# Kernel tuning notes

Hardware: AMD Instinct MI355X
Metric: run time of the kernel (lower is better)

## Reference

```python
import jax, jax.numpy as jnp
import numpy as np

# Dims matching init_kwargs
B, S, D = 2, 2048, 1024
H, E, P, K = 8, 8, 128, 2
SCALE = 1.0 / np.sqrt(P)  # registered buffer 'scale'


def setup_inputs() -> dict:
    key = jax.random.key(0)
    ks = jax.random.split(key, 8)
    std = 1.0 / np.sqrt(D)  # reset_parameters uses std_scale/sqrt(input_size)
    return {
        "x": jax.random.normal(ks[0], (B, S, D), jnp.float32),
        "q_w": jax.random.normal(ks[1], (H * P, D), jnp.float32) * std,
        "k_w": jax.random.normal(ks[2], (H * P, D), jnp.float32) * std,
        "v_w": jax.random.normal(ks[3], (H * E, D, P), jnp.float32) * std,
        "o_w": jax.random.normal(ks[4], (H * E, P, D), jnp.float32) * (1.0 / np.sqrt(H * P)),
        "sel_v_w": jax.random.normal(ks[5], (H * E, D), jnp.float32) * std,
        "sel_o_w": jax.random.normal(ks[6], (H * E, D), jnp.float32) * std,
        "route_scale": jnp.ones((1,), jnp.float32),
    }


def _get_sel_gate(x, w, route_scale):
    """Faithful port of SwitchHeadCore.get_sel (eval mode, no bias):
    sigmoid routing logits per head, top-k expert selection, weight
    normalization, route_scale. Returned as a dense [B,S,H,E] gate so the
    indexed expert combine is expressed as a gated einsum (same math)."""
    logits = jnp.einsum('bsd,ed->bse', x, w).astype(jnp.float32)
    raw = logits.reshape(x.shape[0], x.shape[1], H, E)
    probs = jax.nn.sigmoid(raw)
    vals, idx = jax.lax.top_k(probs, K)                 # [B,S,H,K]
    vals = vals / jnp.clip(vals.sum(-1, keepdims=True), 1e-9)  # normalize_weights
    vals = vals * route_scale
    gate = (jax.nn.one_hot(idx, E, dtype=vals.dtype) * vals[..., None]).sum(-2)
    return gate  # [B,S,H,E]


def reference(x, q_w, k_w, v_w, o_w, sel_v_w, sel_o_w, route_scale):
    rs = route_scale[0]
    gate_v = _get_sel_gate(x, sel_v_w, rs)  # [B,S,H,E]
    gate_o = _get_sel_gate(x, sel_o_w, rs)  # [B,S,H,E]

    # q/k projections -> torch head order [B,H,S,P]
    q = jnp.einsum('bsd,hpd->bhsp', x, q_w.reshape(H, P, D))
    k = jnp.einsum('bsd,hpd->bhsp', x, k_w.reshape(H, P, D))

    # Per-token expert V projection: mixture of selected expert weight slices
    xv = jnp.einsum('bsd,hedp->bshep', x, v_w.reshape(H, E, D, P))
    v = jnp.einsum('bshep,bshe->bhsp', xv, gate_v)

    # Scaled dot-product attention (eval: no dropout)
    att = jax.nn.softmax(jnp.einsum('bhqp,bhkp->bhqk', q, k) * SCALE, axis=-1)
    ctx = jnp.einsum('bhqk,bhkp->bqhp', att, v)  # [B,S,H,P]

    # Per-token expert O projection, gated, summed over heads
    weighted = ctx[:, :, :, None, :] * gate_o[..., None]  # [B,S,H,E,P]
    out = jnp.einsum('bshep,hepd->bsd', weighted, o_w.reshape(H, E, P, D))
    return out
```

## Files before the change

kernel.cpp:

```cpp
#include <hip/hip_runtime.h>


typedef unsigned short u16;
typedef __attribute__((ext_vector_type(8))) short s8v;
typedef __attribute__((ext_vector_type(4))) float f4v;
typedef __attribute__((ext_vector_type(4))) unsigned short us4;

#define ATT_SCALE 0.08838834764831845f

__device__ inline u16 bf16_rne(float f) {
  union { float f; unsigned u; } v; v.f = f;
  unsigned r = v.u + 0x7fffu + ((v.u >> 16) & 1u);
  return (u16)(r >> 16);
}
__device__ inline float bf2f(u16 h) {
  union { unsigned u; float f; } v; v.u = ((unsigned)h) << 16;
  return v.f;
}

__device__ inline void glds16(const void* g, void* l) {
  __builtin_amdgcn_global_load_lds((const __attribute__((address_space(1))) void*)g,
                                   (__attribute__((address_space(3))) void*)l, 16, 0, 0);
}
__device__ inline int swzcol(int idx) {
  int r = idx >> 2;
  return (((idx & 3) ^ ((r + (r >> 2)) & 3)) << 3);
}
#define WAITB() do { asm volatile("s_waitcnt vmcnt(0)" ::: "memory"); __syncthreads(); } while (0)

__global__ void conv_qk(const float* __restrict__ Q, const float* __restrict__ K,
                        u16* __restrict__ Qb, u16* __restrict__ Kb) {
  int i = blockIdx.x * 256 + threadIdx.x;
  const float* src; u16* dst; int off;
  if (i < 262144) { src = Q; dst = Qb; off = i; }
  else            { src = K; dst = Kb; off = i - 262144; }
  float4 v = *(const float4*)&src[(size_t)off * 4];
  us4 o; o[0]=bf16_rne(v.x); o[1]=bf16_rne(v.y); o[2]=bf16_rne(v.z); o[3]=bf16_rne(v.w);
  *(us4*)&dst[(size_t)off * 4] = o;
}

__global__ void transpose_w(const float* __restrict__ src, u16* __restrict__ dst, int mode) {
  __shared__ float tile[32][33];
  int he = blockIdx.z;
  int C = mode ? 1024 : 128;
  int r0 = blockIdx.y * 32, c0 = blockIdx.x * 32;
  int lc = threadIdx.x & 31, rr = threadIdx.x >> 5;
  const float* s = src + (size_t)he * 131072;
#pragma unroll
  for (int i = 0; i < 4; ++i) {
    int r = rr + i * 8;
    tile[r][lc] = s[(size_t)(r0 + r) * C + c0 + lc];
  }
  __syncthreads();
#pragma unroll
  for (int i = 0; i < 4; ++i) {
    int c = rr + i * 8;
    float v = tile[lc][c];
    size_t a;
    if (mode) a = (size_t)(c0 + c) * 8192 + (size_t)he * 128 + (r0 + lc);
    else      a = (size_t)(he >> 3) * 1048576 + (size_t)(c0 + c) * 8192 + (size_t)(he & 7) * 1024 + (r0 + lc);
    dst[a] = bf16_rne(v);
  }
}

__global__ __launch_bounds__(256, 2) void routing(
    const float* __restrict__ X, const float* __restrict__ SelV, const float* __restrict__ SelO,
    const float* __restrict__ RS, int2* __restrict__ Tvi, float2* __restrict__ Tvg,
    int2* __restrict__ Toi, float2* __restrict__ Tog, u16* __restrict__ Xb) {
  __shared__ float xs[8][1024];
  __shared__ float lgs[8][128];
  int t0 = blockIdx.x * 8;
  int tid = threadIdx.x;
  for (int i = tid; i < 2048; i += 256) {
    int row = i >> 8, c = (i & 255) * 4;
    float4 v = *(const float4*)&X[(size_t)(t0 + row) * 1024 + c];
    *(float4*)&xs[row][c] = v;
    us4 o; o[0]=bf16_rne(v.x); o[1]=bf16_rne(v.y); o[2]=bf16_rne(v.z); o[3]=bf16_rne(v.w);
    *(us4*)&Xb[(size_t)(t0 + row) * 1024 + c] = o;
  }
  __syncthreads();
  {
    int widx = tid & 127, tg = tid >> 7;
    const float* w = (widx < 64) ? (SelV + (size_t)widx * 1024) : (SelO + (size_t)(widx - 64) * 1024);
    float acc[4] = {0.f, 0.f, 0.f, 0.f};
    for (int k = 0; k < 1024; k += 4) {
      float4 wv = *(const float4*)&w[k];
#pragma unroll
      for (int t = 0; t < 4; ++t) {
        float4 xv = *(const float4*)&xs[tg * 4 + t][k];
        acc[t] += wv.x * xv.x + wv.y * xv.y + wv.z * xv.z + wv.w * xv.w;
      }
    }
#pragma unroll
    for (int t = 0; t < 4; ++t) lgs[tg * 4 + t][widx] = acc[t];
  }
  __syncthreads();
  if (tid < 128) {
    float rs = RS[0];
    int tok = tid >> 4, which = (tid >> 3) & 1, h = tid & 7;
    float p[8];
#pragma unroll
    for (int e = 0; e < 8; ++e)
      p[e] = 1.f / (1.f + __expf(-lgs[tok][which * 64 + h * 8 + e]));
    float v1 = -1.f; int i1 = -1;
#pragma unroll
    for (int e = 0; e < 8; ++e) if (p[e] > v1) { v1 = p[e]; i1 = e; }
    float v2 = -1.f; int i2 = -1;
#pragma unroll
    for (int e = 0; e < 8; ++e) if (e != i1 && p[e] > v2) { v2 = p[e]; i2 = e; }
    float ssum = fmaxf(v1 + v2, 1e-9f);
    float g1 = v1 / ssum * rs, g2 = v2 / ssum * rs;
    int t = t0 + tok;
    int lo, hi; float glo, ghi;
    if (i1 < i2) { lo = i1; hi = i2; glo = g1; ghi = g2; }
    else         { lo = i2; hi = i1; glo = g2; ghi = g1; }
    if (which) { Toi[t * 8 + h] = make_int2(lo, hi); Tog[t * 8 + h] = make_float2(glo, ghi); }
    else       { Tvi[t * 8 + h] = make_int2(lo, hi); Tvg[t * 8 + h] = make_float2(glo, ghi); }
  }
}

__global__ void build_buckets(const int2* __restrict__ Tvi, const float2* __restrict__ Tvg,
                              int* __restrict__ bcnt, u16* __restrict__ btok,
                              float2* __restrict__ bgate) {
  int t = blockIdx.x * 256 + threadIdx.x;
#pragma unroll
  for (int h = 0; h < 8; ++h) {
    int2 e = Tvi[t * 8 + h];
    int pid = e.x * 7 - (e.x * (e.x - 1)) / 2 + (e.y - e.x - 1);
    int b = h * 28 + pid;
    int pos = atomicAdd(&bcnt[b], 1);
    if (pos < 1024) { btok[b * 1024 + pos] = (u16)t; bgate[b * 1024 + pos] = Tvg[t * 8 + h]; }
  }
}

__global__ __launch_bounds__(256) void gemm_qk(
    const u16* __restrict__ Xb, const u16* __restrict__ Wq, const u16* __restrict__ Wk,
    u16* __restrict__ Qo, u16* __restrict__ Ko) {
  __shared__ u16 Ash0[64 * 32], Ash1[64 * 32];
  __shared__ u16 Bsh0[128 * 32], Bsh1[128 * 32];
  const int tb = blockIdx.x, nb = blockIdx.y;
  const u16* W = blockIdx.z ? Wk : Wq;
  u16* Out = blockIdx.z ? Ko : Qo;
  const int tid = threadIdx.x;
  const int wave = tid >> 6, lane = tid & 63;
  const int lg = lane >> 4, lr = lane & 15;
  const int r0 = tid >> 2, r1 = (tid + 256) >> 2;
  const int c0 = swzcol(tid), c1 = swzcol(tid + 256);
  const size_t aw  = (size_t)(tb * 64 + r0) * 1024 + c0;
  const size_t bw0 = (size_t)(nb * 128 + r0) * 1024 + c0;
  const size_t bw1 = (size_t)(nb * 128 + r1) * 1024 + c1;
  const int csl = (lg ^ ((lr + (lr >> 2)) & 3)) << 3;
  f4v acc[4][2] = {};
#define STG_QK(A, B, k0) do { \
    glds16(&Xb[aw + (k0)], &A[tid * 8]); \
    glds16(&W[bw0 + (k0)], &B[tid * 8]); \
    glds16(&W[bw1 + (k0)], &B[(tid + 256) * 8]); \
  } while (0)
#define CMP_QK(A, B) do { \
    s8v af[4], bfr[2]; \
    _Pragma("unroll") for (int m = 0; m < 4; ++m) af[m] = *(const s8v*)&A[(m * 16 + lr) * 32 + csl]; \
    _Pragma("unroll") for (int n = 0; n < 2; ++n) bfr[n] = *(const s8v*)&B[(wave * 32 + n * 16 + lr) * 32 + csl]; \
    _Pragma("unroll") for (int m = 0; m < 4; ++m) \
      _Pragma("unroll") for (int n = 0; n < 2; ++n) \
        acc[m][n] = __builtin_amdgcn_mfma_f32_16x16x32_bf16(af[m], bfr[n], acc[m][n], 0, 0, 0); \
  } while (0)
  STG_QK(Ash0, Bsh0, 0);
  for (int kt = 0; kt < 32; kt += 2) {
    WAITB();
    if (kt + 1 < 32) STG_QK(Ash1, Bsh1, (kt + 1) * 32);
    CMP_QK(Ash0, Bsh0);
    WAITB();
    if (kt + 2 < 32) STG_QK(Ash0, Bsh0, (kt + 2) * 32);
    CMP_QK(Ash1, Bsh1);
  }
#undef STG_QK
#undef CMP_QK
#pragma unroll
  for (int m = 0; m < 4; ++m) {
    int tbase = tb * 64 + m * 16 + lg * 4;
    int b = tbase >> 11, s = tbase & 2047;
#pragma unroll
    for (int n = 0; n < 2; ++n) {
      int p = wave * 32 + n * 16 + lr;
      size_t base = ((size_t)(b * 8 + nb) * 2048 + s) * 128 + p;
#pragma unroll
      for (int j = 0; j < 4; ++j)
        Out[base + (size_t)j * 128] = bf16_rne(acc[m][n][j]);
    }
  }
}

__global__ __launch_bounds__(256) void gemm_v_sparse(
    const u16* __restrict__ Xb, const u16* __restrict__ Vw ,
    const int* __restrict__ bcnt, const u16* __restrict__ btok,
    const float2* __restrict__ bgate, u16* __restrict__ Vtmp) {
  const int bucket = blockIdx.y;
  const int h = bucket / 28, pid = bucket % 28;
  const int cnt = min(bcnt[bucket], 512);
  const int tile = blockIdx.x;
  if (tile * 64 >= cnt) return;
  int lo = 0, rem = pid;
  while (rem >= 7 - lo) { rem -= 7 - lo; lo++; }
  const int hi = lo + 1 + rem;
  __shared__ u16 Ash0[64 * 32], Ash1[64 * 32];
  __shared__ u16 BL0[128 * 32], BL1[128 * 32];
  __shared__ u16 BH0[128 * 32], BH1[128 * 32];
  __shared__ int toksh[64];
  __shared__ float g0sh[64], g1sh[64];
  const int tid = threadIdx.x;
  if (tid < 64) {
    int ar = tile * 64 + tid;
    if (ar < cnt) {
      toksh[tid] = btok[bucket * 1024 + ar];
      float2 g = bgate[bucket * 1024 + ar];
      g0sh[tid] = g.x; g1sh[tid] = g.y;
    } else { toksh[tid] = 0; g0sh[tid] = 0.f; g1sh[tid] = 0.f; }
  }
  __syncthreads();
  const int wave = tid >> 6, lane = tid & 63;
  const int lg = lane >> 4, lr = lane & 15;
  const int r0 = tid >> 2, r1 = (tid + 256) >> 2;
  const int c0 = swzcol(tid), c1 = swzcol(tid + 256);
  const int tokA = toksh[r0];
  const size_t aw   = (size_t)tokA * 1024 + c0;
  const size_t bwL0 = ((size_t)(h * 128 + r0) * 8 + lo) * 1024 + c0;
  const size_t bwL1 = ((size_t)(h * 128 + r1) * 8 + lo) * 1024 + c1;
  const size_t bwH0 = ((size_t)(h * 128 + r0) * 8 + hi) * 1024 + c0;
  const size_t bwH1 = ((size_t)(h * 128 + r1) * 8 + hi) * 1024 + c1;
  const int csl = (lg ^ ((lr + (lr >> 2)) & 3)) << 3;
  f4v accL[4][2] = {};
  f4v accH[4][2] = {};
#define STG_V(A, BL, BH, d0) do { \
    glds16(&Xb[aw + (d0)], &A[tid * 8]); \
    glds16(&Vw[bwL0 + (d0)], &BL[tid * 8]); \
    glds16(&Vw[bwL1 + (d0)], &BL[(tid + 256) * 8]); \
    glds16(&Vw[bwH0 + (d0)], &BH[tid * 8]); \
    glds16(&Vw[bwH1 + (d0)], &BH[(tid + 256) * 8]); \
  } while (0)
#define CMP_V(A, BL, BH) do { \
    s8v af[4], bl[2], bh[2]; \
    _Pragma("unroll") for (int m = 0; m < 4; ++m) af[m] = *(const s8v*)&A[(m * 16 + lr) * 32 + csl]; \
    _Pragma("unroll") for (int n = 0; n < 2; ++n) { \
      bl[n] = *(const s8v*)&BL[(wave * 32 + n * 16 + lr) * 32 + csl]; \
      bh[n] = *(const s8v*)&BH[(wave * 32 + n * 16 + lr) * 32 + csl]; \
    } \
    _Pragma("unroll") for (int m = 0; m < 4; ++m) \
      _Pragma("unroll") for (int n = 0; n < 2; ++n) { \
        accL[m][n] = __builtin_amdgcn_mfma_f32_16x16x32_bf16(af[m], bl[n], accL[m][n], 0, 0, 0); \
        accH[m][n] = __builtin_amdgcn_mfma_f32_16x16x32_bf16(af[m], bh[n], accH[m][n], 0, 0, 0); \
      } \
  } while (0)
  STG_V(Ash0, BL0, BH0, 0);
  for (int kt = 0; kt < 32; kt += 2) {
    WAITB();
    if (kt + 1 < 32) STG_V(Ash1, BL1, BH1, (kt + 1) * 32);
    CMP_V(Ash0, BL0, BH0);
    WAITB();
    if (kt + 2 < 32) STG_V(Ash0, BL0, BH0, (kt + 2) * 32);
    CMP_V(Ash1, BL1, BH1);
  }
#undef STG_V
#undef CMP_V
#pragma unroll
  for (int m = 0; m < 4; ++m) {
#pragma unroll
    for (int j = 0; j < 4; ++j) {
      int row = m * 16 + lg * 4 + j;
      int ar = tile * 64 + row;
      if (ar < cnt) {
        int tok = toksh[row];
        float g0 = g0sh[row], g1 = g1sh[row];
#pragma unroll
        for (int n = 0; n < 2; ++n) {
          int p = wave * 32 + n * 16 + lr;
          Vtmp[(size_t)tok * 1024 + h * 128 + p] = bf16_rne(g0 * accL[m][n][j] + g1 * accH[m][n][j]);
        }
      }
    }
  }
}

__global__ void vtranspose(const u16* __restrict__ Vtmp, u16* __restrict__ VT) {
  __shared__ u16 tile[64][136];
  const int sb = blockIdx.x, bh = blockIdx.y;
  const int b = bh >> 3, h = bh & 7;
  const int tid = threadIdx.x;
#pragma unroll
  for (int it = 0; it < 4; ++it) {
    int idx = tid + it * 256;
    int r = idx >> 4, c8 = (idx & 15) << 3;
    *(s8v*)&tile[r][c8] = *(const s8v*)&Vtmp[(size_t)(b * 2048 + sb * 64 + r) * 1024 + h * 128 + c8];
  }
  __syncthreads();
#pragma unroll
  for (int it = 0; it < 8; ++it) {
    int idx = tid + it * 256;
    int p = idx >> 4, c4 = (idx & 15) << 2;
    us4 o;
#pragma unroll
    for (int j = 0; j < 4; ++j) o[j] = tile[c4 + j][p];
    *(us4*)&VT[((size_t)bh * 128 + p) * 2048 + sb * 64 + c4] = o;
  }
}

__global__ __launch_bounds__(256, 2) void attn(
    const u16* __restrict__ Q, const u16* __restrict__ K,
    const u16* __restrict__ VT, u16* __restrict__ CTX) {
  __shared__ u16 Kt[64 * 136];
  __shared__ u16 Vt[128 * 72];
  __shared__ u16 Pl[4][16 * 72];
  const int qb = blockIdx.x, bh = blockIdx.y;
  const int tid = threadIdx.x;
  const int wave = tid >> 6, lane = tid & 63;
  const int lg = lane >> 4, lr = lane & 15;
  const size_t base = (size_t)bh * 2048 * 128;
  const int q0 = qb * 64 + wave * 16;
  s8v qf[4];
#pragma unroll
  for (int ks = 0; ks < 4; ++ks)
    qf[ks] = *(const s8v*)&Q[base + (size_t)(q0 + lr) * 128 + ks * 32 + lg * 8];
  f4v cacc[8] = {};
  float mrun = -1e30f, ssum = 0.f;
  for (int kb = 0; kb < 32; ++kb) {
    __syncthreads();
#pragma unroll
    for (int i = 0; i < 4; ++i) {
      int idx = tid + i * 256;
      int r = idx >> 4, c8 = (idx & 15) << 3;
      *(s8v*)&Kt[r * 136 + c8] = *(const s8v*)&K[base + (size_t)(kb * 64 + r) * 128 + c8];
    }
#pragma unroll
    for (int i = 0; i < 4; ++i) {
      int idx = tid + i * 256;
      int r = idx >> 3, c8 = (idx & 7) << 3;
      *(s8v*)&Vt[r * 72 + c8] = *(const s8v*)&VT[base + (size_t)r * 2048 + kb * 64 + c8];
    }
    __syncthreads();
    f4v sc[4] = {};
#pragma unroll
    for (int ks = 0; ks < 4; ++ks) {
#pragma unroll
      for (int m = 0; m < 4; ++m) {
        s8v ak = *(const s8v*)&Kt[(m * 16 + lr) * 136 + ks * 32 + lg * 8];
        sc[m] = __builtin_amdgcn_mfma_f32_16x16x32_bf16(ak, qf[ks], sc[m], 0, 0, 0);
      }
    }
    float tmax = -1e30f;
#pragma unroll
    for (int m = 0; m < 4; ++m)
#pragma unroll
      for (int j = 0; j < 4; ++j) {
        float v = sc[m][j] * ATT_SCALE;
        sc[m][j] = v;
        tmax = fmaxf(tmax, v);
      }
    tmax = fmaxf(tmax, __shfl_xor(tmax, 16));
    tmax = fmaxf(tmax, __shfl_xor(tmax, 32));
    float mnew = fmaxf(mrun, tmax);
    float f = __expf(mrun - mnew);
    mrun = mnew;
    float psum = 0.f;
#pragma unroll
    for (int m = 0; m < 4; ++m) {
      us4 pk;
#pragma unroll
      for (int j = 0; j < 4; ++j) {
        float pe = __expf(sc[m][j] - mnew);
        psum += pe;
        pk[j] = bf16_rne(pe);
      }
      *(us4*)&Pl[wave][lr * 72 + m * 16 + lg * 4] = pk;
    }
    psum += __shfl_xor(psum, 16);
    psum += __shfl_xor(psum, 32);
    ssum = ssum * f + psum;
#pragma unroll
    for (int mr = 0; mr < 8; ++mr)
#pragma unroll
      for (int j = 0; j < 4; ++j) cacc[mr][j] *= f;
#pragma unroll
    for (int ks = 0; ks < 2; ++ks) {
      s8v bp = *(const s8v*)&Pl[wave][lr * 72 + ks * 32 + lg * 8];
#pragma unroll
      for (int mr = 0; mr < 8; ++mr) {
        s8v av = *(const s8v*)&Vt[(mr * 16 + lr) * 72 + ks * 32 + lg * 8];
        cacc[mr] = __builtin_amdgcn_mfma_f32_16x16x32_bf16(av, bp, cacc[mr], 0, 0, 0);
      }
    }
  }
  float rinv = 1.f / ssum;
#pragma unroll
  for (int mr = 0; mr < 8; ++mr) {
    us4 pk;
#pragma unroll
    for (int j = 0; j < 4; ++j) pk[j] = bf16_rne(cacc[mr][j] * rinv);
    *(us4*)&CTX[base + (size_t)(q0 + lr) * 128 + mr * 16 + lg * 4] = pk;
  }
}

__global__ __launch_bounds__(256) void pregate(
    const u16* __restrict__ CTX, const int2* __restrict__ Toi, const float2* __restrict__ Tog,
    u16* __restrict__ CTXG) {
  const int t = blockIdx.x;
  const int tid = threadIdx.x;
  __shared__ float gsh[64];
  if (tid < 64) {
    int h = tid >> 3, e = tid & 7;
    int2 ei = Toi[t * 8 + h];
    float2 gg = Tog[t * 8 + h];
    gsh[tid] = (e == ei.x) ? gg.x : ((e == ei.y) ? gg.y : 0.f);
  }
  __syncthreads();
  const int b = t >> 11, s = t & 2047;
#pragma unroll
  for (int c = 0; c < 4; ++c) {
    int chunk = tid + c * 256;
    int he = chunk >> 4, p8 = (chunk & 15) << 3;
    int h = he >> 3;
    float g = gsh[he];
    s8v o;
    if (g != 0.f) {
      s8v v = *(const s8v*)&CTX[((size_t)(b * 8 + h) * 2048 + s) * 128 + p8];
#pragma unroll
      for (int j = 0; j < 8; ++j) o[j] = (short)bf16_rne(bf2f((u16)v[j]) * g);
    } else {
#pragma unroll
      for (int j = 0; j < 8; ++j) o[j] = 0;
    }
    *(s8v*)&CTXG[(size_t)t * 8192 + chunk * 8] = o;
  }
}

__global__ __launch_bounds__(256) void gemm_o_dense(
    const u16* __restrict__ CTXG, const u16* __restrict__ Ow ,
    float* __restrict__ OUT, float* __restrict__ OP1a, float* __restrict__ OP1b) {
  __shared__ u16 Ash0[128 * 32], Ash1[128 * 32];
  __shared__ u16 Bsh0[128 * 32], Bsh1[128 * 32];
  const int tb = blockIdx.x, db = blockIdx.y, kz = blockIdx.z;
  const int tid = threadIdx.x;
  const int wave = tid >> 6, lane = tid & 63;
  const int wm = wave >> 1, wn = wave & 1;
  const int lg = lane >> 4, lr = lane & 15;
  const size_t kbase = (size_t)kz * 4096;
  const int r0 = tid >> 2, r1 = (tid + 256) >> 2;
  const int c0 = swzcol(tid), c1 = swzcol(tid + 256);
  const size_t aw0 = (size_t)(tb * 128 + r0) * 8192 + kbase + c0;
  const size_t aw1 = (size_t)(tb * 128 + r1) * 8192 + kbase + c1;
  const size_t bw0 = (size_t)(db * 128 + r0) * 8192 + kbase + c0;
  const size_t bw1 = (size_t)(db * 128 + r1) * 8192 + kbase + c1;
  const int csl = (lg ^ ((lr + (lr >> 2)) & 3)) << 3;
  f4v acc[4][4] = {};
#define STG_O(A, B, k0) do { \
    glds16(&CTXG[aw0 + (k0)], &A[tid * 8]); \
    glds16(&CTXG[aw1 + (k0)], &A[(tid + 256) * 8]); \
    glds16(&Ow[bw0 + (k0)], &B[tid * 8]); \
    glds16(&Ow[bw1 + (k0)], &B[(tid + 256) * 8]); \
  } while (0)
#define CMP_O(A, B) do { \
    s8v af[4], bfr[4]; \
    _Pragma("unroll") for (int m = 0; m < 4; ++m) af[m] = *(const s8v*)&A[(wm * 64 + m * 16 + lr) * 32 + csl]; \
    _Pragma("unroll") for (int n = 0; n < 4; ++n) bfr[n] = *(const s8v*)&B[(wn * 64 + n * 16 + lr) * 32 + csl]; \
    _Pragma("unroll") for (int m = 0; m < 4; ++m) \
      _Pragma("unroll") for (int n = 0; n < 4; ++n) \
        acc[m][n] = __builtin_amdgcn_mfma_f32_16x16x32_bf16(af[m], bfr[n], acc[m][n], 0, 0, 0); \
  } while (0)
  STG_O(Ash0, Bsh0, 0);
  for (int kt = 0; kt < 128; kt += 2) {
    WAITB();
    if (kt + 1 < 128) STG_O(Ash1, Bsh1, (kt + 1) * 32);
    CMP_O(Ash0, Bsh0);
    WAITB();
    if (kt + 2 < 128) STG_O(Ash0, Bsh0, (kt + 2) * 32);
    CMP_O(Ash1, Bsh1);
  }
#undef STG_O
#undef CMP_O
  float* OP;
  if (kz == 0) OP = OUT;
  else OP = (tb < 16) ? OP1a : OP1b;
  const int toff = (kz == 0) ? tb * 128 : (tb & 15) * 128;
#pragma unroll
  for (int m = 0; m < 4; ++m) {
    int t = toff + wm * 64 + m * 16 + lg * 4;
#pragma unroll
    for (int n = 0; n < 4; ++n) {
      int d = db * 128 + wn * 64 + n * 16 + lr;
#pragma unroll
      for (int j = 0; j < 4; ++j)
        OP[(size_t)(t + j) * 1024 + d] = acc[m][n][j];
    }
  }
}

__global__ void add_inplace(float* __restrict__ OUT, const float* __restrict__ P0,
                            const float* __restrict__ P1) {
  size_t i = ((size_t)blockIdx.x * 256 + threadIdx.x) * 4;
  const float* P = (i < 2097152) ? (P0 + i) : (P1 + (i - 2097152));
  float4 a = *(const float4*)&OUT[i];
  float4 b = *(const float4*)P;
  *(float4*)&OUT[i] = make_float4(a.x + b.x, a.y + b.y, a.z + b.z, a.w + b.w);
}

extern "C" void kernel_launch(void* const* d_in, const int* in_sizes, int n_in,
                              void* d_out, int out_size, void* d_ws, size_t ws_size,
                              hipStream_t stream) {
  const float* x     = (const float*)d_in[0];
  const float* q_w   = (const float*)d_in[1];
  const float* k_w   = (const float*)d_in[2];
  const float* v_w   = (const float*)d_in[3];
  const float* o_w   = (const float*)d_in[4];
  const float* sel_v = (const float*)d_in[5];
  const float* sel_o = (const float*)d_in[6];
  const float* rs    = (const float*)d_in[7];

  char* ws = (char*)d_ws;
  const size_t MB = 1048576;
  const size_t KB = 1024;
  u16*    xb    = (u16*)(ws);
  u16*    ctx   = (u16*)(ws);
  float*  op1a  = (float*)(ws);
  u16*    qwb   = (u16*)(ws + 8 * MB);
  u16*    kwb   = (u16*)(ws + 10 * MB);
  u16*    ctxg  = (u16*)(ws + 8 * MB);
  u16*    vwT   = (u16*)(ws + 12 * MB);
  u16*    vt    = (u16*)(ws + 12 * MB);
  u16*    vtmp  = (u16*)(ws + 49 * MB + 512 * KB);
  u16*    qh    = (u16*)(ws + 49 * MB + 512 * KB);
  u16*    kh    = (u16*)(ws + 57 * MB + 512 * KB);
  int2*   tvi   = (int2*)(ws + 72 * MB);
  float2* tvg   = (float2*)(ws + 72 * MB + 256 * KB);
  int2*   toi   = (int2*)(ws + 72 * MB + 512 * KB);
  float2* tog   = (float2*)(ws + 72 * MB + 768 * KB);
  int*    bcntv = (int*)(ws + 73 * MB);
  u16*    btokv = (u16*)(ws + 73 * MB + 8 * KB);
  float2* bgatev= (float2*)(ws + 73 * MB + 512 * KB);
  float*  op1b  = (float*)(ws + 72 * MB);
  u16*    owT   = (u16*)(ws + 80 * MB);
  float*  outp  = (float*)d_out;

  hipLaunchKernelGGL(conv_qk, dim3(2048), dim3(256), 0, stream, q_w, k_w, qwb, kwb);
  hipLaunchKernelGGL(transpose_w, dim3(4, 32, 64), dim3(256), 0, stream, v_w, vwT, 0);
  hipLaunchKernelGGL(transpose_w, dim3(32, 4, 64), dim3(256), 0, stream, o_w, owT, 1);
  hipMemsetAsync(bcntv, 0, 4 * KB, stream);
  hipLaunchKernelGGL(routing, dim3(512), dim3(256), 0, stream, x, sel_v, sel_o, rs, tvi, tvg, toi, tog, xb);
  hipLaunchKernelGGL(build_buckets, dim3(16), dim3(256), 0, stream, tvi, tvg, bcntv, btokv, bgatev);
  hipLaunchKernelGGL(gemm_v_sparse, dim3(8, 224), dim3(256), 0, stream, xb, vwT, bcntv, btokv, bgatev, vtmp);
  hipLaunchKernelGGL(vtranspose, dim3(32, 16), dim3(256), 0, stream, vtmp, vt);
  hipLaunchKernelGGL(gemm_qk, dim3(64, 8, 2), dim3(256), 0, stream, xb, qwb, kwb, qh, kh);
  hipLaunchKernelGGL(attn, dim3(32, 16), dim3(256), 0, stream, qh, kh, vt, ctx);
  hipLaunchKernelGGL(pregate, dim3(4096), dim3(256), 0, stream, ctx, toi, tog, ctxg);
  hipLaunchKernelGGL(gemm_o_dense, dim3(32, 8, 2), dim3(256), 0, stream, ctxg, owT, outp, op1a, op1b);
  hipLaunchKernelGGL(add_inplace, dim3(4096), dim3(256), 0, stream, outp, op1a, op1b);
}
```

Measured before the change: 424.3 us.

## Bucket V projection per expert with 128-token tiles and add partials in transpose

The sparse V projection now groups tokens by single expert (8 buckets per head) instead of by expert pair (28 buckets per head). Each block computes a 128x128 tile for one expert, and the routing gate is applied at store time. Each token's two expert contributions go to separate buffers (A or B, chosen by a flag bit in the token index), and the transpose kernel sums them. The aim is denser buckets and less padded-tile waste, plus better operand reuse from the larger tile. The cost is an extra 8MB of bf16 partials written and read, and rounding each partial to bf16 before the add.

```diff
diff --git a/kernel.cpp b/kernel.cpp
--- a/kernel.cpp
+++ b/kernel.cpp
@@ -119,17 +119,22 @@
   }
 }
 
-__global__ void build_buckets(const int2* __restrict__ Tvi, const float2* __restrict__ Tvg,
-                              int* __restrict__ bcnt, u16* __restrict__ btok,
-                              float2* __restrict__ bgate) {
+__global__ void build_buckets2(const int2* __restrict__ Tvi, const float2* __restrict__ Tvg,
+                               int* __restrict__ bcnt, u16* __restrict__ btok,
+                               float* __restrict__ bgate) {
   int t = blockIdx.x * 256 + threadIdx.x;
 #pragma unroll
   for (int h = 0; h < 8; ++h) {
     int2 e = Tvi[t * 8 + h];
-    int pid = e.x * 7 - (e.x * (e.x - 1)) / 2 + (e.y - e.x - 1);
-    int b = h * 28 + pid;
-    int pos = atomicAdd(&bcnt[b], 1);
-    if (pos < 1024) { btok[b * 1024 + pos] = (u16)t; bgate[b * 1024 + pos] = Tvg[t * 8 + h]; }
+    float2 g = Tvg[t * 8 + h];
+    int bA = h * 8 + e.x;
+    int pA = atomicAdd(&bcnt[bA], 1);
+    btok[bA * 4096 + pA] = (u16)t;
+    bgate[bA * 4096 + pA] = g.x;
+    int bB = h * 8 + e.y;
+    int pB = atomicAdd(&bcnt[bB], 1);
+    btok[bB * 4096 + pB] = (u16)(t | 0x8000);
+    bgate[bB * 4096 + pB] = g.y;
   }
 }
 
@@ -190,97 +195,87 @@
   }
 }
 
-__global__ __launch_bounds__(256) void gemm_v_sparse(
+__global__ __launch_bounds__(256) void gemm_v_e(
     const u16* __restrict__ Xb, const u16* __restrict__ Vw ,
     const int* __restrict__ bcnt, const u16* __restrict__ btok,
-    const float2* __restrict__ bgate, u16* __restrict__ Vtmp) {
+    const float* __restrict__ bgate, u16* __restrict__ VpA, u16* __restrict__ VpB) {
   const int bucket = blockIdx.y;
-  const int h = bucket / 28, pid = bucket % 28;
-  const int cnt = min(bcnt[bucket], 512);
+  const int h = bucket >> 3, e = bucket & 7;
+  const int cnt = bcnt[bucket];
   const int tile = blockIdx.x;
-  if (tile * 64 >= cnt) return;
-  int lo = 0, rem = pid;
-  while (rem >= 7 - lo) { rem -= 7 - lo; lo++; }
-  const int hi = lo + 1 + rem;
-  __shared__ u16 Ash0[64 * 32], Ash1[64 * 32];
-  __shared__ u16 BL0[128 * 32], BL1[128 * 32];
-  __shared__ u16 BH0[128 * 32], BH1[128 * 32];
-  __shared__ int toksh[64];
-  __shared__ float g0sh[64], g1sh[64];
+  if (tile * 128 >= cnt) return;
+  __shared__ u16 Ash0[128 * 32], Ash1[128 * 32];
+  __shared__ u16 Bsh0[128 * 32], Bsh1[128 * 32];
+  __shared__ int toksh[128];
+  __shared__ float gsh[128];
   const int tid = threadIdx.x;
-  if (tid < 64) {
-    int ar = tile * 64 + tid;
+  if (tid < 128) {
+    int ar = tile * 128 + tid;
     if (ar < cnt) {
-      toksh[tid] = btok[bucket * 1024 + ar];
-      float2 g = bgate[bucket * 1024 + ar];
-      g0sh[tid] = g.x; g1sh[tid] = g.y;
-    } else { toksh[tid] = 0; g0sh[tid] = 0.f; g1sh[tid] = 0.f; }
+      toksh[tid] = btok[bucket * 4096 + ar];
+      gsh[tid] = bgate[bucket * 4096 + ar];
+    } else { toksh[tid] = 0; gsh[tid] = 0.f; }
   }
   __syncthreads();
   const int wave = tid >> 6, lane = tid & 63;
+  const int wm = wave >> 1, wn = wave & 1;
   const int lg = lane >> 4, lr = lane & 15;
   const int r0 = tid >> 2, r1 = (tid + 256) >> 2;
   const int c0 = swzcol(tid), c1 = swzcol(tid + 256);
-  const int tokA = toksh[r0];
-  const size_t aw   = (size_t)tokA * 1024 + c0;
-  const size_t bwL0 = ((size_t)(h * 128 + r0) * 8 + lo) * 1024 + c0;
-  const size_t bwL1 = ((size_t)(h * 128 + r1) * 8 + lo) * 1024 + c1;
-  const size_t bwH0 = ((size_t)(h * 128 + r0) * 8 + hi) * 1024 + c0;
-  const size_t bwH1 = ((size_t)(h * 128 + r1) * 8 + hi) * 1024 + c1;
+  const size_t aw0 = (size_t)(toksh[r0] & 0xFFF) * 1024 + c0;
+  const size_t aw1 = (size_t)(toksh[r1] & 0xFFF) * 1024 + c1;
+  const size_t bw0 = ((size_t)(h * 128 + r0) * 8 + e) * 1024 + c0;
+  const size_t bw1 = ((size_t)(h * 128 + r1) * 8 + e) * 1024 + c1;
   const int csl = (lg ^ ((lr + (lr >> 2)) & 3)) << 3;
-  f4v accL[4][2] = {};
-  f4v accH[4][2] = {};
-#define STG_V(A, BL, BH, d0) do { \
-    glds16(&Xb[aw + (d0)], &A[tid * 8]); \
-    glds16(&Vw[bwL0 + (d0)], &BL[tid * 8]); \
-    glds16(&Vw[bwL1 + (d0)], &BL[(tid + 256) * 8]); \
-    glds16(&Vw[bwH0 + (d0)], &BH[tid * 8]); \
-    glds16(&Vw[bwH1 + (d0)], &BH[(tid + 256) * 8]); \
+  f4v acc[4][4] = {};
+#define STG_VE(A, B, k0) do { \
+    glds16(&Xb[aw0 + (k0)], &A[tid * 8]); \
+    glds16(&Xb[aw1 + (k0)], &A[(tid + 256) * 8]); \
+    glds16(&Vw[bw0 + (k0)], &B[tid * 8]); \
+    glds16(&Vw[bw1 + (k0)], &B[(tid + 256) * 8]); \
   } while (0)
-#define CMP_V(A, BL, BH) do { \
-    s8v af[4], bl[2], bh[2]; \
-    _Pragma("unroll") for (int m = 0; m < 4; ++m) af[m] = *(const s8v*)&A[(m * 16 + lr) * 32 + csl]; \
-    _Pragma("unroll") for (int n = 0; n < 2; ++n) { \
-      bl[n] = *(const s8v*)&BL[(wave * 32 + n * 16 + lr) * 32 + csl]; \
-      bh[n] = *(const s8v*)&BH[(wave * 32 + n * 16 + lr) * 32 + csl]; \
-    } \
+#define CMP_VE(A, B) do { \
+    s8v af[4], bfr[4]; \
+    _Pragma("unroll") for (int m = 0; m < 4; ++m) af[m] = *(const s8v*)&A[(wm * 64 + m * 16 + lr) * 32 + csl]; \
+    _Pragma("unroll") for (int n = 0; n < 4; ++n) bfr[n] = *(const s8v*)&B[(wn * 64 + n * 16 + lr) * 32 + csl]; \
     _Pragma("unroll") for (int m = 0; m < 4; ++m) \
-      _Pragma("unroll") for (int n = 0; n < 2; ++n) { \
-        accL[m][n] = __builtin_amdgcn_mfma_f32_16x16x32_bf16(af[m], bl[n], accL[m][n], 0, 0, 0); \
-        accH[m][n] = __builtin_amdgcn_mfma_f32_16x16x32_bf16(af[m], bh[n], accH[m][n], 0, 0, 0); \
-      } \
+      _Pragma("unroll") for (int n = 0; n < 4; ++n) \
+        acc[m][n] = __builtin_amdgcn_mfma_f32_16x16x32_bf16(af[m], bfr[n], acc[m][n], 0, 0, 0); \
   } while (0)
-  STG_V(Ash0, BL0, BH0, 0);
+  STG_VE(Ash0, Bsh0, 0);
   for (int kt = 0; kt < 32; kt += 2) {
     WAITB();
-    if (kt + 1 < 32) STG_V(Ash1, BL1, BH1, (kt + 1) * 32);
-    CMP_V(Ash0, BL0, BH0);
+    if (kt + 1 < 32) STG_VE(Ash1, Bsh1, (kt + 1) * 32);
+    CMP_VE(Ash0, Bsh0);
     WAITB();
-    if (kt + 2 < 32) STG_V(Ash0, BL0, BH0, (kt + 2) * 32);
-    CMP_V(Ash1, BL1, BH1);
-  }
-#undef STG_V
-#undef CMP_V
+    if (kt + 2 < 32) STG_VE(Ash0, Bsh0, (kt + 2) * 32);
+    CMP_VE(Ash1, Bsh1);
+  }
+#undef STG_VE
+#undef CMP_VE
 #pragma unroll
   for (int m = 0; m < 4; ++m) {
 #pragma unroll
     for (int j = 0; j < 4; ++j) {
-      int row = m * 16 + lg * 4 + j;
-      int ar = tile * 64 + row;
+      int row = wm * 64 + m * 16 + lg * 4 + j;
+      int ar = tile * 128 + row;
       if (ar < cnt) {
-        int tok = toksh[row];
-        float g0 = g0sh[row], g1 = g1sh[row];
-#pragma unroll
-        for (int n = 0; n < 2; ++n) {
-          int p = wave * 32 + n * 16 + lr;
-          Vtmp[(size_t)tok * 1024 + h * 128 + p] = bf16_rne(g0 * accL[m][n][j] + g1 * accH[m][n][j]);
+        int entry = toksh[row];
+        int tok = entry & 0xFFF;
+        u16* dst = (entry & 0x8000) ? VpB : VpA;
+        float g = gsh[row];
+#pragma unroll
+        for (int n = 0; n < 4; ++n) {
+          int p = wn * 64 + n * 16 + lr;
+          dst[(size_t)tok * 1024 + h * 128 + p] = bf16_rne(g * acc[m][n][j]);
         }
       }
     }
   }
 }
 
-__global__ void vtranspose(const u16* __restrict__ Vtmp, u16* __restrict__ VT) {
+__global__ void vadd_transpose(const u16* __restrict__ VpA, const u16* __restrict__ VpB,
+                               u16* __restrict__ VT) {
   __shared__ u16 tile[64][136];
   const int sb = blockIdx.x, bh = blockIdx.y;
   const int b = bh >> 3, h = bh & 7;
@@ -289,7 +284,13 @@
   for (int it = 0; it < 4; ++it) {
     int idx = tid + it * 256;
     int r = idx >> 4, c8 = (idx & 15) << 3;
-    *(s8v*)&tile[r][c8] = *(const s8v*)&Vtmp[(size_t)(b * 2048 + sb * 64 + r) * 1024 + h * 128 + c8];
+    size_t off = (size_t)(b * 2048 + sb * 64 + r) * 1024 + h * 128 + c8;
+    s8v va = *(const s8v*)&VpA[off];
+    s8v vb = *(const s8v*)&VpB[off];
+    s8v o;
+#pragma unroll
+    for (int j = 0; j < 8; ++j) o[j] = (short)bf16_rne(bf2f((u16)va[j]) + bf2f((u16)vb[j]));
+    *(s8v*)&tile[r][c8] = o;
   }
   __syncthreads();
 #pragma unroll
@@ -524,16 +525,17 @@
   u16*    ctxg  = (u16*)(ws + 8 * MB);
   u16*    vwT   = (u16*)(ws + 12 * MB);
   u16*    vt    = (u16*)(ws + 12 * MB);
-  u16*    vtmp  = (u16*)(ws + 49 * MB + 512 * KB);
+  u16*    vpA   = (u16*)(ws + 28 * MB);
+  u16*    vpB   = (u16*)(ws + 36 * MB);
   u16*    qh    = (u16*)(ws + 49 * MB + 512 * KB);
   u16*    kh    = (u16*)(ws + 57 * MB + 512 * KB);
   int2*   tvi   = (int2*)(ws + 72 * MB);
   float2* tvg   = (float2*)(ws + 72 * MB + 256 * KB);
   int2*   toi   = (int2*)(ws + 72 * MB + 512 * KB);
   float2* tog   = (float2*)(ws + 72 * MB + 768 * KB);
-  int*    bcntv = (int*)(ws + 73 * MB);
-  u16*    btokv = (u16*)(ws + 73 * MB + 8 * KB);
-  float2* bgatev= (float2*)(ws + 73 * MB + 512 * KB);
+  int*    bcnt2 = (int*)(ws + 73 * MB);
+  u16*    btok2 = (u16*)(ws + 73 * MB + 4 * KB);
+  float*  bgate2= (float*)(ws + 73 * MB + 520 * KB);
   float*  op1b  = (float*)(ws + 72 * MB);
   u16*    owT   = (u16*)(ws + 80 * MB);
   float*  outp  = (float*)d_out;
@@ -541,11 +543,11 @@
   hipLaunchKernelGGL(conv_qk, dim3(2048), dim3(256), 0, stream, q_w, k_w, qwb, kwb);
   hipLaunchKernelGGL(transpose_w, dim3(4, 32, 64), dim3(256), 0, stream, v_w, vwT, 0);
   hipLaunchKernelGGL(transpose_w, dim3(32, 4, 64), dim3(256), 0, stream, o_w, owT, 1);
-  hipMemsetAsync(bcntv, 0, 4 * KB, stream);
+  hipMemsetAsync(bcnt2, 0, 4 * KB, stream);
   hipLaunchKernelGGL(routing, dim3(512), dim3(256), 0, stream, x, sel_v, sel_o, rs, tvi, tvg, toi, tog, xb);
-  hipLaunchKernelGGL(build_buckets, dim3(16), dim3(256), 0, stream, tvi, tvg, bcntv, btokv, bgatev);
-  hipLaunchKernelGGL(gemm_v_sparse, dim3(8, 224), dim3(256), 0, stream, xb, vwT, bcntv, btokv, bgatev, vtmp);
-  hipLaunchKernelGGL(vtranspose, dim3(32, 16), dim3(256), 0, stream, vtmp, vt);
+  hipLaunchKernelGGL(build_buckets2, dim3(16), dim3(256), 0, stream, tvi, tvg, bcnt2, btok2, bgate2);
+  hipLaunchKernelGGL(gemm_v_e, dim3(32, 64), dim3(256), 0, stream, xb, vwT, bcnt2, btok2, bgate2, vpA, vpB);
+  hipLaunchKernelGGL(vadd_transpose, dim3(32, 16), dim3(256), 0, stream, vpA, vpB, vt);
   hipLaunchKernelGGL(gemm_qk, dim3(64, 8, 2), dim3(256), 0, stream, xb, qwb, kwb, qh, kh);
   hipLaunchKernelGGL(attn, dim3(32, 16), dim3(256), 0, stream, qh, kh, vt, ctx);
   hipLaunchKernelGGL(pregate, dim3(4096), dim3(256), 0, stream, ctx, toi, tog, ctxg);
```

After: 645.5 us. 1.52x slower.
